# Optimization experiments

Hardware: AMD Instinct MI355X
Metric: run time of the kernel (lower is better)

The kernel has to match this reference:

```python
import jax, jax.numpy as jnp
import numpy as np

EMBED_DIM = 256
N_LEVELS = 4
N_HEADS = 8
N_POINTS = 4
HEAD_DIM = EMBED_DIM // N_HEADS
N_QUERIES = 8192
BATCH = 2
LEVEL_SHAPES = np.array([[128, 128], [64, 64], [32, 32], [16, 16]], dtype=np.int32)
HMAX, WMAX = 128, 128
EPS = 1e-5


def setup_inputs() -> dict:
    key = jax.random.key(0)
    ks = jax.random.split(key, 10)
    scale = 1.0 / np.sqrt(EMBED_DIM)
    query = jax.random.normal(ks[0], (N_QUERIES, EMBED_DIM), jnp.float32)
    xy_reference_points = jax.random.uniform(ks[1], (N_QUERIES, 2), jnp.float32, 0.05, 0.95)
    val = jax.random.normal(ks[2], (BATCH, HMAX, WMAX, N_LEVELS, EMBED_DIM), jnp.float32)
    # zero outside each level's valid support (mimics sparse COO: absent entries read as 0)
    hh = jnp.arange(HMAX)[:, None, None]
    ww = jnp.arange(WMAX)[None, :, None]
    lh = jnp.asarray(LEVEL_SHAPES[:, 0])[None, None, :]
    lw = jnp.asarray(LEVEL_SHAPES[:, 1])[None, None, :]
    mask = ((hh < lh) & (ww < lw)).astype(jnp.float32)
    stacked_value_tensors = val * mask[None, :, :, :, None]
    return {
        "query": query,
        "xy_reference_points": xy_reference_points,
        "stacked_value_tensors": stacked_value_tensors,
        "W_off": (jax.random.normal(ks[3], (EMBED_DIM, N_LEVELS * N_POINTS * N_HEADS * 2)) * scale * 0.1).astype(jnp.float32),
        "b_off": (jax.random.normal(ks[4], (N_LEVELS * N_POINTS * N_HEADS * 2,)) * 0.5).astype(jnp.float32),
        "W_attn": (jax.random.normal(ks[5], (EMBED_DIM, N_LEVELS * N_POINTS * N_HEADS)) * scale).astype(jnp.float32),
        "b_attn": jnp.zeros((N_LEVELS * N_POINTS * N_HEADS,), jnp.float32),
        "W_out": (jax.random.normal(ks[6], (EMBED_DIM, EMBED_DIM)) * scale).astype(jnp.float32),
        "b_out": jnp.zeros((EMBED_DIM,), jnp.float32),
        "batch_offsets": jnp.array([0, N_QUERIES // 2], jnp.int32),
        "spatial_shapes": jnp.asarray(LEVEL_SHAPES, jnp.int32),
    }


def reference(query, xy_reference_points, stacked_value_tensors, W_off, b_off,
              W_attn, b_attn, W_out, b_out, batch_offsets, spatial_shapes):
    Q = query.shape[0]
    # sampling offsets & attention weights (torch Linear with W stored [in,out])
    off = (query @ W_off + b_off).reshape(Q, N_LEVELS, N_POINTS, N_HEADS, 2)
    aw = (query @ W_attn + b_attn).reshape(Q, N_LEVELS * N_POINTS, N_HEADS)
    aw = jax.nn.softmax(aw, axis=1).reshape(Q, N_LEVELS, N_POINTS, N_HEADS)
    # sampling locations: sigmoid(inverse_sigmoid(ref) + offsets), then map (0,1)->(-1,1)
    r = jnp.clip(xy_reference_points, 0.0, 1.0)
    inv = jnp.log(jnp.clip(r, EPS, 1.0) / jnp.clip(1.0 - r, EPS, 1.0))
    loc = jax.nn.sigmoid(inv[:, None, None, None, :] + off) * 2.0 - 1.0  # (Q,L,P,H,2)
    # per-query batch index from batch_offsets (start index per batch element)
    bidx = jnp.searchsorted(batch_offsets, jnp.arange(Q), side="right") - 1  # (Q,)
    b = bidx[:, None, None, None]
    h_sz = spatial_shapes[:, 0].astype(loc.dtype)[None, :, None, None]
    w_sz = spatial_shapes[:, 1].astype(loc.dtype)[None, :, None, None]
    x = ((loc[..., 0] + 1.0) * w_sz - 1.0) / 2.0  # (Q,L,P,H)
    y = ((loc[..., 1] + 1.0) * h_sz - 1.0) / 2.0
    x0 = jnp.floor(x).astype(jnp.int32); x1 = x0 + 1
    y0 = jnp.floor(y).astype(jnp.int32); y1 = y0 + 1
    wcap = (spatial_shapes[:, 1] - 1).astype(jnp.int32)[None, :, None, None]
    hcap = (spatial_shapes[:, 0] - 1).astype(jnp.int32)[None, :, None, None]
    x0 = jnp.clip(x0, 0, wcap); x1 = jnp.clip(x1, 0, wcap)
    y0 = jnp.clip(y0, 0, hcap); y1 = jnp.clip(y1, 0, hcap)
    x0f = x0.astype(x.dtype); x1f = x1.astype(x.dtype)
    y0f = y0.astype(y.dtype); y1f = y1.astype(y.dtype)
    wa = (x1f - x) * (y1f - y)  # pairs with (x0,y0), as in source
    wb = (x1f - x) * (y - y0f)  # (x0,y1)
    wc = (x - x0f) * (y1f - y)  # (x1,y0)
    wd = (x - x0f) * (y - y0f)  # (x1,y1)
    V = stacked_value_tensors.reshape(BATCH, HMAX, WMAX, N_LEVELS, N_HEADS, HEAD_DIM)
    l = jnp.arange(N_LEVELS)[None, :, None, None]
    h = jnp.arange(N_HEADS)[None, None, None, :]
    # NOTE: source indexes (batch, x, y, level, head) -> x indexes the height dim; levels are square
    def g(xi, yi):
        return V[b, xi, yi, l, h]  # (Q,L,P,H,HEAD_DIM)
    sampled = (wa[..., None] * g(x0, y0) + wb[..., None] * g(x0, y1)
               + wc[..., None] * g(x1, y0) + wd[..., None] * g(x1, y1))
    out = jnp.einsum("qlphd,qlph->qhd", sampled, aw).reshape(Q, EMBED_DIM)
    return out @ W_out + b_out
```

## Files before the change

kernel.cpp:

```cpp
#include <hip/hip_runtime.h>
#include <math.h>

#define ED      256
#define NL      4
#define NH      8
#define NP      4
#define HD      32
#define HMAX    128
#define WMAX    128
#define NLP     16
#define NC      128
#define NOFF_AW 384
#define QPB     8
#define BSTRIDE (HMAX*WMAX*NL*ED)
#define XSTRIDE (WMAX*NL*ED)
#define YSTRIDE (NL*ED)
#define RPB     21760
#define PBC     (RPB*256)

typedef __attribute__((ext_vector_type(8))) __fp16   f16x8;
typedef __attribute__((ext_vector_type(4))) __fp16   f16x4;
typedef __attribute__((ext_vector_type(4))) float    f32x4;

__constant__ int LBASE_ROW[4] = {0, 16384, 20480, 21504};

__global__ __launch_bounds__(1024) void msda_prep_kernel(
    const float* __restrict__ V,
    const float* __restrict__ W_off,
    const float* __restrict__ W_attn,
    const float* __restrict__ W_out,
    __fp16* __restrict__ Vc,
    __fp16* __restrict__ WcatT,
    __fp16* __restrict__ WoutT,
    int nb, int nCompact)
{
    const int bid = blockIdx.x;
    const int t   = threadIdx.x;

    if (bid < nCompact) {
        const int r    = bid * 16 + (t >> 6);
        const int lane = t & 63;
        const int h    = lane >> 3;
        const int j4   = lane & 7;
        const int total_rows = nb * RPB;
        if (r < total_rows) {
            const int b  = r / RPB;
            const int rr = r - b * RPB;
            int l;
            if (rr < 16384)      { l = 0; }
            else if (rr < 20480) { l = 1; }
            else if (rr < 21504) { l = 2; }
            else                 { l = 3; }
            const int pos = rr - LBASE_ROW[l];
            const int lsh = 7 - l;
            const int xi  = pos >> lsh;
            const int yi  = pos & ((1 << lsh) - 1);
            const int plane32 = (1 << (2 * lsh)) * 32;
            const float4 src = *(const float4*)&V[(size_t)b * BSTRIDE +
                (size_t)xi * XSTRIDE + (size_t)yi * YSTRIDE + l * ED +
                h * HD + j4 * 4];
            f16x4 d;
            d[0] = (__fp16)src.x; d[1] = (__fp16)src.y;
            d[2] = (__fp16)src.z; d[3] = (__fp16)src.w;
            const size_t dst = (size_t)b * PBC + (size_t)LBASE_ROW[l] * 256 +
                               (size_t)h * plane32 + (size_t)pos * 32 + j4 * 4;
            *(f16x4*)&Vc[dst] = d;
        }
    } else {
        const int idx = (bid - nCompact) * 1024 + t;
        const int t2 = NOFF_AW * ED;
        const int t3 = ED * ED;
        if (idx < t2) {
            int c = idx >> 8, e = idx & 255;
            float v = (c < ED) ? W_off[e * ED + c] : W_attn[e * NC + (c - ED)];
            WcatT[idx] = (__fp16)v;
        } else if (idx < t2 + t3) {
            int i = idx - t2;
            int c = i >> 8, e = i & 255;
            WoutT[i] = (__fp16)W_out[e * ED + c];
        }
    }
}

__global__ __launch_bounds__(256) void gemm_f16_kernel(
    const float*  __restrict__ A,
    const __fp16* __restrict__ BT,
    const float* __restrict__ bias0,
    const float* __restrict__ bias1,
    float* __restrict__ C,
    int M, int NTOT, int bias_split)
{
    const int wave = threadIdx.x >> 6;
    const int lane = threadIdx.x & 63;
    const int gw   = blockIdx.x * 4 + wave;
    const int ngroups = NTOT >> 6;
    const int mg = gw / ngroups, ng = gw % ngroups;
    const int m16 = mg * 16, n64 = ng * 64;
    if (m16 >= M) return;

    const int mrow = lane & 15;
    const int quad = lane >> 4;

    const float4* Arow = (const float4*)(A + (size_t)(m16 + mrow) * 256 + quad * 8);
    const f16x8* B0 = (const f16x8*)(BT + (size_t)(n64 +  0 + mrow) * 256 + quad * 8);
    const f16x8* B1 = (const f16x8*)(BT + (size_t)(n64 + 16 + mrow) * 256 + quad * 8);
    const f16x8* B2 = (const f16x8*)(BT + (size_t)(n64 + 32 + mrow) * 256 + quad * 8);
    const f16x8* B3 = (const f16x8*)(BT + (size_t)(n64 + 48 + mrow) * 256 + quad * 8);

    f32x4 acc0 = {0.f,0.f,0.f,0.f}, acc1 = acc0, acc2 = acc0, acc3 = acc0;
    #pragma unroll
    for (int kb = 0; kb < 8; ++kb) {
        float4 a0 = Arow[kb * 8 + 0];
        float4 a1 = Arow[kb * 8 + 1];
        float av[8] = {a0.x, a0.y, a0.z, a0.w, a1.x, a1.y, a1.z, a1.w};
        f16x8 ah, al;
        #pragma unroll
        for (int j = 0; j < 8; ++j) {
            __fp16 h = (__fp16)av[j];
            ah[j] = h;
            al[j] = (__fp16)(av[j] - (float)h);
        }
        f16x8 b0 = B0[kb * 4], b1 = B1[kb * 4], b2 = B2[kb * 4], b3 = B3[kb * 4];
        acc0 = __builtin_amdgcn_mfma_f32_16x16x32_f16(ah, b0, acc0, 0, 0, 0);
        acc1 = __builtin_amdgcn_mfma_f32_16x16x32_f16(ah, b1, acc1, 0, 0, 0);
        acc2 = __builtin_amdgcn_mfma_f32_16x16x32_f16(ah, b2, acc2, 0, 0, 0);
        acc3 = __builtin_amdgcn_mfma_f32_16x16x32_f16(ah, b3, acc3, 0, 0, 0);
        acc0 = __builtin_amdgcn_mfma_f32_16x16x32_f16(al, b0, acc0, 0, 0, 0);
        acc1 = __builtin_amdgcn_mfma_f32_16x16x32_f16(al, b1, acc1, 0, 0, 0);
        acc2 = __builtin_amdgcn_mfma_f32_16x16x32_f16(al, b2, acc2, 0, 0, 0);
        acc3 = __builtin_amdgcn_mfma_f32_16x16x32_f16(al, b3, acc3, 0, 0, 0);
    }

    const int col = lane & 15;
    f32x4 accs[4] = {acc0, acc1, acc2, acc3};
    #pragma unroll
    for (int i = 0; i < 4; ++i) {
        int n = n64 + i * 16 + col;
        float b = (n < bias_split) ? bias0[n] : bias1[n - bias_split];
        #pragma unroll
        for (int r = 0; r < 4; ++r) {
            int row = m16 + quad * 4 + r;
            C[(size_t)row * NTOT + n] = accs[i][r] + b;
        }
    }
}

__global__ __launch_bounds__(512) void msda_sample_kernel(
    const float*  __restrict__ refp,
    const __fp16* __restrict__ Vc,
    const float*  __restrict__ off_aw,
    const int*    __restrict__ batch_off,
    int n_batch,
    const __fp16* __restrict__ WoutT,
    const float*  __restrict__ b_out,
    float* __restrict__ out,
    int q_total)
{
    __shared__ float  law[QPB][NC];
    __shared__ float2 sminv[QPB][NH];
    __shared__ float2 sref[QPB];
    __shared__ int2   soff[QPB][NC];
    __shared__ float4 swt[QPB][NC];
    __shared__ __attribute__((aligned(16))) __fp16 sout[16][ED + 8];

    const int t  = threadIdx.x;
    const int q0 = blockIdx.x * QPB;

    if (t < 264) {
        f16x8 z = {};
        ((f16x8*)&sout[QPB][0])[t] = z;
    }

    {
        const int s = t >> 6, c = t & 63;
        const float* row = off_aw + (size_t)(q0 + s) * NOFF_AW + ED;
        law[s][c]      = row[c];
        law[s][c + 64] = row[c + 64];
    }
    __syncthreads();

    if (t < QPB * NH) {
        const int s = t >> 3, h = t & 7;
        float m = -1e30f;
        #pragma unroll
        for (int lp = 0; lp < NLP; ++lp) m = fmaxf(m, law[s][lp * NH + h]);
        float sum = 0.f;
        #pragma unroll
        for (int lp = 0; lp < NLP; ++lp) sum += __expf(law[s][lp * NH + h] - m);
        sminv[s][h] = make_float2(m, 1.f / sum);
    } else if (t < QPB * NH + QPB) {
        const int s = t - QPB * NH;
        const int qid = q0 + s;
        float rx = refp[qid * 2 + 0], ry = refp[qid * 2 + 1];
        rx = fminf(fmaxf(rx, 0.f), 1.f);
        ry = fminf(fmaxf(ry, 0.f), 1.f);
        float ivx = __logf(fmaxf(rx, 1e-5f) / fmaxf(1.f - rx, 1e-5f));
        float ivy = __logf(fmaxf(ry, 1e-5f) / fmaxf(1.f - ry, 1e-5f));
        sref[s] = make_float2(ivx, ivy);
    }
    __syncthreads();

    {
        const int s = t >> 6;
        const int qid = q0 + s;
        int b = 0;
        for (int i = 1; i < n_batch; ++i)
            if (batch_off[i] <= qid) b = i;
        const int cb = b * PBC;
        const float2 iv = sref[s];
        const float* offrow = off_aw + (size_t)qid * NOFF_AW;

        #pragma unroll
        for (int half = 0; half < 2; ++half) {
            const int c = (t & 63) + half * 64;
            const int l = c >> 5;
            const int lsh = 7 - l;
            const int sz  = 1 << lsh;
            const int cap = sz - 1;
            const int h = c & 7;
            const int plane32 = (sz * sz) << 5;

            const float2 mi = sminv[s][h];
            const float a = __expf(law[s][c] - mi.x) * mi.y;

            const float ox = offrow[c * 2 + 0], oy = offrow[c * 2 + 1];
            float lx = 2.f / (1.f + __expf(-(iv.x + ox))) - 1.f;
            float ly = 2.f / (1.f + __expf(-(iv.y + oy))) - 1.f;
            float x = ((lx + 1.f) * (float)sz - 1.f) * 0.5f;
            float y = ((ly + 1.f) * (float)sz - 1.f) * 0.5f;
            int x0 = (int)floorf(x), y0 = (int)floorf(y);
            int x1 = x0 + 1, y1 = y0 + 1;
            x0 = min(max(x0, 0), cap); x1 = min(max(x1, 0), cap);
            y0 = min(max(y0, 0), cap); y1 = min(max(y1, 0), cap);
            float x0f = (float)x0, x1f = (float)x1;
            float y0f = (float)y0, y1f = (float)y1;

            float w00 = a * (x1f - x) * (y1f - y);
            float w01 = a * (x1f - x) * (y - y0f);
            float w10 = a * (x - x0f) * (y1f - y);
            float w11 = a * (x - x0f) * (y - y0f);
            if (y1 == y0) {
                w00 += w01; w01 = 0.f;
                w10 += w11; w11 = 0.f;
            }
            swt[s][c] = make_float4(w00, w01, w10, w11);
            const int lb = cb + (LBASE_ROW[l] << 8) + h * plane32;
            int2 o;
            o.x = lb + (((x0 << lsh) + y0) << 5);
            o.y = lb + (((x1 << lsh) + y0) << 5);
            soff[s][c] = o;
        }
    }
    __syncthreads();

    {
        const int s    = t >> 6;
        const int lane = t & 63;
        const int h    = lane >> 3;
        const int j    = lane & 7;
        const int top  = j >> 2;
        const int blk  = j & 3;

        float acc[8];
        #pragma unroll
        for (int k = 0; k < 8; ++k) acc[k] = 0.f;

        #pragma unroll 4
        for (int lp = 0; lp < NLP; ++lp) {
            const int c = lp * NH + h;
            int2   o = soff[s][c];
            float4 w = swt[s][c];
            f16x8 va = *(const f16x8*)&Vc[o.x + j * 8];
            f16x8 vb = *(const f16x8*)&Vc[o.y + j * 8];
            const float wa = top ? w.y : w.x;
            const float wb = top ? w.w : w.z;
            #pragma unroll
            for (int k = 0; k < 8; ++k)
                acc[k] += wa * (float)va[k] + wb * (float)vb[k];
        }
        #pragma unroll
        for (int k = 0; k < 8; ++k)
            acc[k] += __shfl_xor(acc[k], 4);

        if (top == 0) {
            f16x8 o8;
            #pragma unroll
            for (int k = 0; k < 8; ++k) o8[k] = (__fp16)acc[k];
            *(f16x8*)&sout[s][h * HD + blk * 8] = o8;
        }
    }
    __syncthreads();

    {
        const int w    = t >> 6;
        const int lane = t & 63;
        const int mrow = lane & 15;
        const int quad = lane >> 4;

        const f16x8* B0 = (const f16x8*)(WoutT + (size_t)(w * 32 +  0 + mrow) * 256 + quad * 8);
        const f16x8* B1 = (const f16x8*)(WoutT + (size_t)(w * 32 + 16 + mrow) * 256 + quad * 8);

        f32x4 acc0 = {0.f,0.f,0.f,0.f}, acc1 = acc0;
        #pragma unroll
        for (int kb = 0; kb < 8; ++kb) {
            f16x8 af = *(const f16x8*)&sout[mrow][quad * 8 + kb * 32];
            acc0 = __builtin_amdgcn_mfma_f32_16x16x32_f16(af, B0[kb * 4], acc0, 0, 0, 0);
            acc1 = __builtin_amdgcn_mfma_f32_16x16x32_f16(af, B1[kb * 4], acc1, 0, 0, 0);
        }

        const int col = lane & 15;
        f32x4 accs[2] = {acc0, acc1};
        #pragma unroll
        for (int i = 0; i < 2; ++i) {
            int n = w * 32 + i * 16 + col;
            float bb = b_out[n];
            #pragma unroll
            for (int r = 0; r < 4; ++r) {
                int row = quad * 4 + r;
                if (row < QPB)
                    out[(size_t)(q0 + row) * ED + n] = accs[i][r] + bb;
            }
        }
    }
}

extern "C" void kernel_launch(void* const* d_in, const int* in_sizes, int n_in,
                              void* d_out, int out_size, void* d_ws, size_t ws_size,
                              hipStream_t stream) {
    const float* query  = (const float*)d_in[0];
    const float* refp   = (const float*)d_in[1];
    const float* V      = (const float*)d_in[2];
    const float* W_off  = (const float*)d_in[3];
    const float* b_off  = (const float*)d_in[4];
    const float* W_attn = (const float*)d_in[5];
    const float* b_attn = (const float*)d_in[6];
    const float* W_out  = (const float*)d_in[7];
    const float* b_out  = (const float*)d_in[8];
    const int*   boff   = (const int*)d_in[9];
    const int n_batch   = in_sizes[9];
    const int nq        = in_sizes[0] / ED;
    const int nb        = in_sizes[2] / BSTRIDE;
    float* out = (float*)d_out;

    char* ws = (char*)d_ws;
    float*   off_aw  = (float*)ws;
    __fp16*  WcatT   = (__fp16*)(off_aw + (size_t)nq * NOFF_AW);
    __fp16*  WoutT   = WcatT + NOFF_AW * ED;
    __fp16*  Vc      = WoutT + ED * ED;

    {
        int nCompact = (nb * RPB + 15) / 16;
        int nWconv   = (NOFF_AW * ED + ED * ED + 1023) / 1024;
        msda_prep_kernel<<<nCompact + nWconv, 1024, 0, stream>>>(
            V, W_off, W_attn, W_out, Vc, WcatT, WoutT, nb, nCompact);
    }
    {
        int waves = (nq / 16) * (NOFF_AW / 64);
        gemm_f16_kernel<<<(waves + 3) / 4, 256, 0, stream>>>(
            query, WcatT, b_off, b_attn, off_aw, nq, NOFF_AW, ED);
    }
    {
        msda_sample_kernel<<<nq / QPB, 512, 0, stream>>>(
            refp, Vc, off_aw, boff, n_batch, WoutT, b_out, out, nq);
    }
}
```

Before: 259.3 us.

## Fuse offset/attention projection GEMM into sampling kernel via shared memory

Removes the separate projection GEMM kernel. Each sampling block now computes its own 8 queries' offset and attention logits with MFMA and keeps them in shared memory, unioned with the output staging buffer. This drops one launch and the global write and read of the off_aw intermediate. In exchange, half of each 16-row MFMA tile is wasted because only 8 queries are valid, WcatT is reloaded by every block, and launch bounds now request a minimum occupancy.

```diff
diff --git a/kernel.cpp b/kernel.cpp
--- a/kernel.cpp
+++ b/kernel.cpp
@@ -82,73 +82,13 @@
     }
 }
 
-__global__ __launch_bounds__(256) void gemm_f16_kernel(
-    const float*  __restrict__ A,
-    const __fp16* __restrict__ BT,
-    const float* __restrict__ bias0,
-    const float* __restrict__ bias1,
-    float* __restrict__ C,
-    int M, int NTOT, int bias_split)
-{
-    const int wave = threadIdx.x >> 6;
-    const int lane = threadIdx.x & 63;
-    const int gw   = blockIdx.x * 4 + wave;
-    const int ngroups = NTOT >> 6;
-    const int mg = gw / ngroups, ng = gw % ngroups;
-    const int m16 = mg * 16, n64 = ng * 64;
-    if (m16 >= M) return;
-
-    const int mrow = lane & 15;
-    const int quad = lane >> 4;
-
-    const float4* Arow = (const float4*)(A + (size_t)(m16 + mrow) * 256 + quad * 8);
-    const f16x8* B0 = (const f16x8*)(BT + (size_t)(n64 +  0 + mrow) * 256 + quad * 8);
-    const f16x8* B1 = (const f16x8*)(BT + (size_t)(n64 + 16 + mrow) * 256 + quad * 8);
-    const f16x8* B2 = (const f16x8*)(BT + (size_t)(n64 + 32 + mrow) * 256 + quad * 8);
-    const f16x8* B3 = (const f16x8*)(BT + (size_t)(n64 + 48 + mrow) * 256 + quad * 8);
-
-    f32x4 acc0 = {0.f,0.f,0.f,0.f}, acc1 = acc0, acc2 = acc0, acc3 = acc0;
-    #pragma unroll
-    for (int kb = 0; kb < 8; ++kb) {
-        float4 a0 = Arow[kb * 8 + 0];
-        float4 a1 = Arow[kb * 8 + 1];
-        float av[8] = {a0.x, a0.y, a0.z, a0.w, a1.x, a1.y, a1.z, a1.w};
-        f16x8 ah, al;
-        #pragma unroll
-        for (int j = 0; j < 8; ++j) {
-            __fp16 h = (__fp16)av[j];
-            ah[j] = h;
-            al[j] = (__fp16)(av[j] - (float)h);
-        }
-        f16x8 b0 = B0[kb * 4], b1 = B1[kb * 4], b2 = B2[kb * 4], b3 = B3[kb * 4];
-        acc0 = __builtin_amdgcn_mfma_f32_16x16x32_f16(ah, b0, acc0, 0, 0, 0);
-        acc1 = __builtin_amdgcn_mfma_f32_16x16x32_f16(ah, b1, acc1, 0, 0, 0);
-        acc2 = __builtin_amdgcn_mfma_f32_16x16x32_f16(ah, b2, acc2, 0, 0, 0);
-        acc3 = __builtin_amdgcn_mfma_f32_16x16x32_f16(ah, b3, acc3, 0, 0, 0);
-        acc0 = __builtin_amdgcn_mfma_f32_16x16x32_f16(al, b0, acc0, 0, 0, 0);
-        acc1 = __builtin_amdgcn_mfma_f32_16x16x32_f16(al, b1, acc1, 0, 0, 0);
-        acc2 = __builtin_amdgcn_mfma_f32_16x16x32_f16(al, b2, acc2, 0, 0, 0);
-        acc3 = __builtin_amdgcn_mfma_f32_16x16x32_f16(al, b3, acc3, 0, 0, 0);
-    }
-
-    const int col = lane & 15;
-    f32x4 accs[4] = {acc0, acc1, acc2, acc3};
-    #pragma unroll
-    for (int i = 0; i < 4; ++i) {
-        int n = n64 + i * 16 + col;
-        float b = (n < bias_split) ? bias0[n] : bias1[n - bias_split];
-        #pragma unroll
-        for (int r = 0; r < 4; ++r) {
-            int row = m16 + quad * 4 + r;
-            C[(size_t)row * NTOT + n] = accs[i][r] + b;
-        }
-    }
-}
-
-__global__ __launch_bounds__(512) void msda_sample_kernel(
+__global__ __launch_bounds__(512, 6) void msda_sample_kernel(
     const float*  __restrict__ refp,
     const __fp16* __restrict__ Vc,
-    const float*  __restrict__ off_aw,
+    const float*  __restrict__ query,
+    const __fp16* __restrict__ WcatT,
+    const float*  __restrict__ b_off,
+    const float*  __restrict__ b_attn,
     const int*    __restrict__ batch_off,
     int n_batch,
     const __fp16* __restrict__ WoutT,
@@ -156,26 +96,64 @@
     float* __restrict__ out,
     int q_total)
 {
-    __shared__ float  law[QPB][NC];
+    __shared__ __attribute__((aligned(16))) union {
+        float  offaw[QPB][NOFF_AW];
+        __fp16 sout[16][ED + 8];
+    } u;
     __shared__ float2 sminv[QPB][NH];
     __shared__ float2 sref[QPB];
     __shared__ int2   soff[QPB][NC];
     __shared__ float4 swt[QPB][NC];
-    __shared__ __attribute__((aligned(16))) __fp16 sout[16][ED + 8];
 
     const int t  = threadIdx.x;
     const int q0 = blockIdx.x * QPB;
-
-    if (t < 264) {
-        f16x8 z = {};
-        ((f16x8*)&sout[QPB][0])[t] = z;
-    }
-
-    {
-        const int s = t >> 6, c = t & 63;
-        const float* row = off_aw + (size_t)(q0 + s) * NOFF_AW + ED;
-        law[s][c]      = row[c];
-        law[s][c + 64] = row[c + 64];
+    const int w    = t >> 6;
+    const int lane = t & 63;
+
+    {
+        const int mrow = lane & 15;
+        const int quad = lane >> 4;
+        const int arow = q0 + (mrow & 7);
+        const float4* Arow = (const float4*)(query + (size_t)arow * 256 + quad * 8);
+        const int nbase = w * 48;
+        const f16x8* B0 = (const f16x8*)(WcatT + (size_t)(nbase +  0 + mrow) * 256 + quad * 8);
+        const f16x8* B1 = (const f16x8*)(WcatT + (size_t)(nbase + 16 + mrow) * 256 + quad * 8);
+        const f16x8* B2 = (const f16x8*)(WcatT + (size_t)(nbase + 32 + mrow) * 256 + quad * 8);
+
+        f32x4 acc0 = {0.f,0.f,0.f,0.f}, acc1 = acc0, acc2 = acc0;
+        #pragma unroll
+        for (int kb = 0; kb < 8; ++kb) {
+            float4 a0 = Arow[kb * 8 + 0];
+            float4 a1 = Arow[kb * 8 + 1];
+            float av[8] = {a0.x, a0.y, a0.z, a0.w, a1.x, a1.y, a1.z, a1.w};
+            f16x8 ah, al;
+            #pragma unroll
+            for (int j = 0; j < 8; ++j) {
+                __fp16 hh = (__fp16)av[j];
+                ah[j] = hh;
+                al[j] = (__fp16)(av[j] - (float)hh);
+            }
+            f16x8 b0 = B0[kb * 4], b1 = B1[kb * 4], b2 = B2[kb * 4];
+            acc0 = __builtin_amdgcn_mfma_f32_16x16x32_f16(ah, b0, acc0, 0, 0, 0);
+            acc1 = __builtin_amdgcn_mfma_f32_16x16x32_f16(ah, b1, acc1, 0, 0, 0);
+            acc2 = __builtin_amdgcn_mfma_f32_16x16x32_f16(ah, b2, acc2, 0, 0, 0);
+            acc0 = __builtin_amdgcn_mfma_f32_16x16x32_f16(al, b0, acc0, 0, 0, 0);
+            acc1 = __builtin_amdgcn_mfma_f32_16x16x32_f16(al, b1, acc1, 0, 0, 0);
+            acc2 = __builtin_amdgcn_mfma_f32_16x16x32_f16(al, b2, acc2, 0, 0, 0);
+        }
+        const int col = lane & 15;
+        f32x4 accs[3] = {acc0, acc1, acc2};
+        #pragma unroll
+        for (int i = 0; i < 3; ++i) {
+            int n = nbase + i * 16 + col;
+            float bb = (n < ED) ? b_off[n] : b_attn[n - ED];
+            #pragma unroll
+            for (int r = 0; r < 4; ++r) {
+                int row = quad * 4 + r;
+                if (row < QPB)
+                    u.offaw[row][n] = accs[i][r] + bb;
+            }
+        }
     }
     __syncthreads();
 
@@ -183,10 +161,12 @@
         const int s = t >> 3, h = t & 7;
         float m = -1e30f;
         #pragma unroll
-        for (int lp = 0; lp < NLP; ++lp) m = fmaxf(m, law[s][lp * NH + h]);
+        for (int lp = 0; lp < NLP; ++lp)
+            m = fmaxf(m, u.offaw[s][ED + lp * NH + h]);
         float sum = 0.f;
         #pragma unroll
-        for (int lp = 0; lp < NLP; ++lp) sum += __expf(law[s][lp * NH + h] - m);
+        for (int lp = 0; lp < NLP; ++lp)
+            sum += __expf(u.offaw[s][ED + lp * NH + h] - m);
         sminv[s][h] = make_float2(m, 1.f / sum);
     } else if (t < QPB * NH + QPB) {
         const int s = t - QPB * NH;
@@ -201,18 +181,18 @@
     __syncthreads();
 
     {
-        const int s = t >> 6;
+        const int s = w;
         const int qid = q0 + s;
         int b = 0;
         for (int i = 1; i < n_batch; ++i)
             if (batch_off[i] <= qid) b = i;
         const int cb = b * PBC;
         const float2 iv = sref[s];
-        const float* offrow = off_aw + (size_t)qid * NOFF_AW;
+        const float* offrow = u.offaw[s];
 
         #pragma unroll
         for (int half = 0; half < 2; ++half) {
-            const int c = (t & 63) + half * 64;
+            const int c = lane + half * 64;
             const int l = c >> 5;
             const int lsh = 7 - l;
             const int sz  = 1 << lsh;
@@ -221,7 +201,7 @@
             const int plane32 = (sz * sz) << 5;
 
             const float2 mi = sminv[s][h];
-            const float a = __expf(law[s][c] - mi.x) * mi.y;
+            const float a = __expf(offrow[ED + c] - mi.x) * mi.y;
 
             const float ox = offrow[c * 2 + 0], oy = offrow[c * 2 + 1];
             float lx = 2.f / (1.f + __expf(-(iv.x + ox))) - 1.f;
@@ -254,8 +234,12 @@
     __syncthreads();
 
     {
-        const int s    = t >> 6;
-        const int lane = t & 63;
+        if (t < 264) {
+            f16x8 z = {};
+            ((f16x8*)&u.sout[QPB][0])[t] = z;
+        }
+
+        const int s    = w;
         const int h    = lane >> 3;
         const int j    = lane & 7;
         const int top  = j >> 2;
@@ -269,11 +253,11 @@
         for (int lp = 0; lp < NLP; ++lp) {
             const int c = lp * NH + h;
             int2   o = soff[s][c];
-            float4 w = swt[s][c];
+            float4 wt = swt[s][c];
             f16x8 va = *(const f16x8*)&Vc[o.x + j * 8];
             f16x8 vb = *(const f16x8*)&Vc[o.y + j * 8];
-            const float wa = top ? w.y : w.x;
-            const float wb = top ? w.w : w.z;
+            const float wa = top ? wt.y : wt.x;
+            const float wb = top ? wt.w : wt.z;
             #pragma unroll
             for (int k = 0; k < 8; ++k)
                 acc[k] += wa * (float)va[k] + wb * (float)vb[k];
@@ -286,14 +270,12 @@
             f16x8 o8;
             #pragma unroll
             for (int k = 0; k < 8; ++k) o8[k] = (__fp16)acc[k];
-            *(f16x8*)&sout[s][h * HD + blk * 8] = o8;
+            *(f16x8*)&u.sout[s][h * HD + blk * 8] = o8;
         }
     }
     __syncthreads();
 
     {
-        const int w    = t >> 6;
-        const int lane = t & 63;
         const int mrow = lane & 15;
         const int quad = lane >> 4;
 
@@ -303,7 +285,7 @@
         f32x4 acc0 = {0.f,0.f,0.f,0.f}, acc1 = acc0;
         #pragma unroll
         for (int kb = 0; kb < 8; ++kb) {
-            f16x8 af = *(const f16x8*)&sout[mrow][quad * 8 + kb * 32];
+            f16x8 af = *(const f16x8*)&u.sout[mrow][quad * 8 + kb * 32];
             acc0 = __builtin_amdgcn_mfma_f32_16x16x32_f16(af, B0[kb * 4], acc0, 0, 0, 0);
             acc1 = __builtin_amdgcn_mfma_f32_16x16x32_f16(af, B1[kb * 4], acc1, 0, 0, 0);
         }
@@ -343,10 +325,9 @@
     float* out = (float*)d_out;
 
     char* ws = (char*)d_ws;
-    float*   off_aw  = (float*)ws;
-    __fp16*  WcatT   = (__fp16*)(off_aw + (size_t)nq * NOFF_AW);
-    __fp16*  WoutT   = WcatT + NOFF_AW * ED;
-    __fp16*  Vc      = WoutT + ED * ED;
+    __fp16*  WcatT = (__fp16*)ws;
+    __fp16*  WoutT = WcatT + NOFF_AW * ED;
+    __fp16*  Vc    = WoutT + ED * ED;
 
     {
         int nCompact = (nb * RPB + 15) / 16;
@@ -355,12 +336,8 @@
             V, W_off, W_attn, W_out, Vc, WcatT, WoutT, nb, nCompact);
     }
     {
-        int waves = (nq / 16) * (NOFF_AW / 64);
-        gemm_f16_kernel<<<(waves + 3) / 4, 256, 0, stream>>>(
-            query, WcatT, b_off, b_attn, off_aw, nq, NOFF_AW, ED);
-    }
-    {
         msda_sample_kernel<<<nq / QPB, 512, 0, stream>>>(
-            refp, Vc, off_aw, boff, n_batch, WoutT, b_out, out, nq);
+            refp, Vc, query, WcatT, b_off, b_attn, boff, n_batch,
+            WoutT, b_out, out, nq);
     }
 }
```

New measurement: 270.7 us. 4.4% more time.
